# Kernel tuning notes

Measured on AMD Instinct MI355X. Metric: run time of the kernel, lower is better.

Reference implementation:

```python
import jax, jax.numpy as jnp
import numpy as np

N_NODES = 50000
N_EDGES = 400000
N_GRAPHS = 128
IN_DIM = 768
HID = 128
N_CLASSES = 11
BN_EPS = 1e-5


def _sage_conv(x, src, dst, Wl, bl, Wr):
    # PyG SAGEConv (aggr='mean'): out = lin_l(mean_{j->i} x_j) + lin_r(x_i)
    # messages flow src -> dst; nodes with no in-edges get a zero aggregate.
    n = x.shape[0]
    deg = jax.ops.segment_sum(jnp.ones_like(dst, x.dtype), dst, num_segments=n)
    agg = jax.ops.segment_sum(x[src], dst, num_segments=n)  # [N, d] gather+scatter
    agg = agg / jnp.maximum(deg, 1.0)[:, None]
    return agg @ Wl.T + bl + x @ Wr.T


def _batch_norm(x, gamma, beta):
    # training-mode BatchNorm1d: biased batch statistics over the node axis
    m = jnp.mean(x, axis=0)
    v = jnp.var(x, axis=0)
    return (x - m) * jax.lax.rsqrt(v + BN_EPS) * gamma + beta


def setup_inputs() -> dict:
    key = jax.random.key(0)
    ks = jax.random.split(key, 16)
    x = jax.random.normal(ks[0], (N_NODES, IN_DIM), dtype=jnp.float32)
    edge_index = jax.random.randint(ks[1], (2, N_EDGES), 0, N_NODES, dtype=jnp.int32)
    batch = jnp.sort(jax.random.randint(ks[2], (N_NODES,), 0, N_GRAPHS, dtype=jnp.int32))

    def lin_w(k, out_d, in_d):
        return jax.random.normal(k, (out_d, in_d), dtype=jnp.float32) * (1.0 / np.sqrt(in_d))

    params = {
        'W1l': lin_w(ks[3], HID, IN_DIM), 'b1': jnp.zeros((HID,), jnp.float32),
        'W1r': lin_w(ks[4], HID, IN_DIM),
        'g1': jnp.ones((HID,), jnp.float32), 'be1': jnp.zeros((HID,), jnp.float32),
        'W2l': lin_w(ks[5], HID, HID), 'b2': jnp.zeros((HID,), jnp.float32),
        'W2r': lin_w(ks[6], HID, HID),
        'g2': jnp.ones((HID,), jnp.float32), 'be2': jnp.zeros((HID,), jnp.float32),
        'W3l': lin_w(ks[7], HID, HID), 'b3': jnp.zeros((HID,), jnp.float32),
        'W3r': lin_w(ks[8], HID, HID),
        'g3': jnp.ones((HID,), jnp.float32), 'be3': jnp.zeros((HID,), jnp.float32),
        'Wlin': lin_w(ks[9], N_CLASSES, HID), 'blin': jnp.zeros((N_CLASSES,), jnp.float32),
    }
    return {'x': x, 'edge_index': edge_index, 'batch': batch, **params}


def reference(x, edge_index, batch,
              W1l, b1, W1r, g1, be1,
              W2l, b2, W2r, g2, be2,
              W3l, b3, W3r, g3, be3,
              Wlin, blin):
    src, dst = edge_index[0], edge_index[1]
    h = jax.nn.relu(_batch_norm(_sage_conv(x, src, dst, W1l, b1, W1r), g1, be1))
    h = jax.nn.relu(_batch_norm(_sage_conv(h, src, dst, W2l, b2, W2r), g2, be2))
    h = _batch_norm(_sage_conv(h, src, dst, W3l, b3, W3r), g3, be3)
    # global_max_pool over graph ids
    pooled = jax.ops.segment_max(h, batch, num_segments=N_GRAPHS)  # [G, HID]
    # dropout is identity at inference
    return pooled @ Wlin.T + blin  # [G, 11]
```

## Files before the change

### kernel.cpp

```cpp
#include <hip/hip_runtime.h>

#define N_NODESC 50000
#define N_EDGESC 400000
#define N_GRAPHSC 128
#define IN_DIMC 768
#define HIDC 128
#define NCLSC 11
#define BN_EPSC 1e-5f
#define NB_AGG 8
#define NREP 64
#define SCAN_NB ((N_NODESC + 255) / 256)

typedef __bf16 bf16_t;
typedef __bf16 bf16x2 __attribute__((ext_vector_type(2)));
typedef __bf16 bf16x8 __attribute__((ext_vector_type(8)));
typedef float f32x4 __attribute__((ext_vector_type(4)));

typedef __attribute__((address_space(1))) void glb_void;
typedef __attribute__((address_space(3))) void lds_void;

__device__ __forceinline__ void cp16(const void* g, void* l) {
    __builtin_amdgcn_global_load_lds((glb_void*)g, (lds_void*)l, 16, 0, 0);
}

__device__ __forceinline__ f32x4 mfma_16x16x32_bf16(bf16x8 a, bf16x8 b, f32x4 c) {
    return __builtin_amdgcn_mfma_f32_16x16x32_bf16(a, b, c, 0, 0, 0);
}

template<int MODE, int KC>
__global__ __launch_bounds__(256) void gemm_kernel(const void* __restrict__ Av,
                                                   const bf16_t* __restrict__ Wb,
                                                   const float* __restrict__ stats,
                                                   const float* __restrict__ g,
                                                   const float* __restrict__ be,
                                                   bf16_t* __restrict__ Cl,
                                                   bf16_t* __restrict__ Cr,
                                                   int M)
{
    constexpr int NK   = KC / 32;
    constexpr int ASZ  = (MODE == 0) ? 16384 : 8192;
    constexpr int BSZ  = 8192;
    constexpr int NAB  = (MODE == 0) ? 2 : 3;
    constexpr int NBB  = (MODE == 0) ? 2 : 3;
    constexpr int AISS = (MODE == 0) ? 4 : 2;
    constexpr int SCSZ = (MODE == 1) ? 1024 : 16;
    __shared__ __align__(16) unsigned char smem[NAB * ASZ + NBB * BSZ + SCSZ];
    unsigned char* Asm = smem;
    unsigned char* Bsm = smem + NAB * ASZ;
    float* scS = (float*)(smem + NAB * ASZ + NBB * BSZ);

    const int bid  = blockIdx.x;
    const int p    = ((bid >> 4) << 3) + (bid & 7);
    const int half = (bid >> 3) & 1;
    if (p * 128 >= M) return;
    const int m0 = p * 128;

    const int t    = threadIdx.x;
    const int wid  = t >> 6;
    const int lane = t & 63;
    const int wm   = (wid >> 1) * 64;
    const int wn   = (wid & 1) * 64;
    const int l16  = lane & 15;
    const int quad = lane >> 4;

    const char* aSrc[AISS]; int aDst[AISS];
#pragma unroll
    for (int s = 0; s < AISS; s++) {
        int L = (s * 4 + wid) * 64 + lane;
        int r, c;
        if (MODE == 0) { r = L >> 3; c = (L & 7) ^ (r & 7); }
        else           { r = L >> 2; c = (L & 3) ^ ((r >> 1) & 3); }
        int row = m0 + r; if (row > M - 1) row = M - 1;
        if (MODE == 0) aSrc[s] = (const char*)Av + ((size_t)row * KC + (size_t)c * 4) * 4;
        else           aSrc[s] = (const char*)Av + ((size_t)row * KC + (size_t)c * 8) * 2;
        aDst[s] = (s * 4 + wid) * 1024;
    }
    const char* bSrc[2]; int bDst[2];
#pragma unroll
    for (int s = 0; s < 2; s++) {
        int L = (s * 4 + wid) * 64 + lane;
        int r = L >> 2;
        int c = (L & 3) ^ ((r >> 1) & 3);
        bSrc[s] = (const char*)(Wb + (size_t)(half * 128 + r) * KC + c * 8);
        bDst[s] = (s * 4 + wid) * 1024;
    }

    int aOff[4][2], bOff[4];
#pragma unroll
    for (int i = 0; i < 4; i++) {
        int ra = wm + i * 16 + l16;
        if (MODE == 0) {
            aOff[i][0] = ra * 128 + (((2 * quad)     ^ (ra & 7)) * 16);
            aOff[i][1] = ra * 128 + (((2 * quad + 1) ^ (ra & 7)) * 16);
        } else {
            aOff[i][0] = ra * 64 + ((quad ^ ((ra >> 1) & 3)) * 16);
            aOff[i][1] = 0;
        }
        int rb = wn + i * 16 + l16;
        bOff[i] = rb * 64 + ((quad ^ ((rb >> 1) & 3)) * 16);
    }

    if (MODE == 1) {
        if (t < HIDC) {
            float sum = 0.f, sumsq = 0.f;
            for (int r = 0; r < NREP; r++) {
                sum   += stats[r * 256 + t];
                sumsq += stats[r * 256 + HIDC + t];
            }
            float invM = 1.0f / (float)M;
            float mean = sum * invM;
            float var  = sumsq * invM - mean * mean;
            float s = rsqrtf(var + BN_EPSC) * g[t];
            scS[t] = s;
            scS[HIDC + t] = be[t] - mean * s;
        }
        __syncthreads();
    }

    f32x4 acc[4][4] = {};

    if constexpr (MODE == 0) {
#pragma unroll
        for (int s = 0; s < 4; s++) cp16(aSrc[s], Asm + aDst[s]);
#pragma unroll
        for (int s = 0; s < 2; s++) cp16(bSrc[s], Bsm + bDst[s]);

        for (int it = 0; it < NK; ++it) {
            if (it + 1 < NK) {
                const size_t ka = (size_t)(it + 1) * 128;
                const size_t kb = (size_t)(it + 1) * 64;
                const int nb = (it + 1) & 1;
#pragma unroll
                for (int s = 0; s < 4; s++) cp16(aSrc[s] + ka, Asm + nb * ASZ + aDst[s]);
#pragma unroll
                for (int s = 0; s < 2; s++) cp16(bSrc[s] + kb, Bsm + nb * BSZ + bDst[s]);
                asm volatile("s_waitcnt vmcnt(6)" ::: "memory");
            } else {
                asm volatile("s_waitcnt vmcnt(0)" ::: "memory");
            }
            asm volatile("s_barrier" ::: "memory");

            const unsigned char* Ab = Asm + (it & 1) * ASZ;
            const unsigned char* Bb = Bsm + (it & 1) * BSZ;
            bf16x8 af[4], bfr[4];
#pragma unroll
            for (int i = 0; i < 4; i++) {
                float4 u0 = *(const float4*)(Ab + aOff[i][0]);
                float4 u1 = *(const float4*)(Ab + aOff[i][1]);
                af[i][0] = (bf16_t)u0.x; af[i][1] = (bf16_t)u0.y;
                af[i][2] = (bf16_t)u0.z; af[i][3] = (bf16_t)u0.w;
                af[i][4] = (bf16_t)u1.x; af[i][5] = (bf16_t)u1.y;
                af[i][6] = (bf16_t)u1.z; af[i][7] = (bf16_t)u1.w;
            }
#pragma unroll
            for (int j = 0; j < 4; j++)
                bfr[j] = *(const bf16x8*)(Bb + bOff[j]);
#pragma unroll
            for (int i = 0; i < 4; i++)
#pragma unroll
                for (int j = 0; j < 4; j++)
                    acc[i][j] = mfma_16x16x32_bf16(af[i], bfr[j], acc[i][j]);

            asm volatile("s_barrier" ::: "memory");
        }
    } else {
#pragma unroll
        for (int s = 0; s < 2; s++) cp16(aSrc[s], Asm + aDst[s]);
#pragma unroll
        for (int s = 0; s < 2; s++) cp16(bSrc[s], Bsm + bDst[s]);
#pragma unroll
        for (int s = 0; s < 2; s++) cp16(aSrc[s] + 64, Asm + ASZ + aDst[s]);
#pragma unroll
        for (int s = 0; s < 2; s++) cp16(bSrc[s] + 64, Bsm + BSZ + bDst[s]);

        for (int it = 0; it < NK; ++it) {
            if (it + 2 < NK) {
                const size_t kb2 = (size_t)(it + 2) * 64;
                const int nb = (it + 2) % 3;
#pragma unroll
                for (int s = 0; s < 2; s++) cp16(aSrc[s] + kb2, Asm + nb * ASZ + aDst[s]);
#pragma unroll
                for (int s = 0; s < 2; s++) cp16(bSrc[s] + kb2, Bsm + nb * BSZ + bDst[s]);
                asm volatile("s_waitcnt vmcnt(8)" ::: "memory");
            } else if (it + 1 < NK) {
                asm volatile("s_waitcnt vmcnt(4)" ::: "memory");
            } else {
                asm volatile("s_waitcnt vmcnt(0)" ::: "memory");
            }
            asm volatile("s_barrier" ::: "memory");

            const unsigned char* Ab = Asm + (it % 3) * ASZ;
            const unsigned char* Bb = Bsm + (it % 3) * BSZ;
            bf16x8 af[4], bfr[4];
            float4 s0 = *(const float4*)&scS[it * 32 + quad * 8];
            float4 s1 = *(const float4*)&scS[it * 32 + quad * 8 + 4];
            float4 h0 = *(const float4*)&scS[HIDC + it * 32 + quad * 8];
            float4 h1 = *(const float4*)&scS[HIDC + it * 32 + quad * 8 + 4];
            float ss[8] = {s0.x, s0.y, s0.z, s0.w, s1.x, s1.y, s1.z, s1.w};
            float hh[8] = {h0.x, h0.y, h0.z, h0.w, h1.x, h1.y, h1.z, h1.w};
#pragma unroll
            for (int i = 0; i < 4; i++) {
                bf16x8 raw = *(const bf16x8*)(Ab + aOff[i][0]);
#pragma unroll
                for (int e = 0; e < 8; e++)
                    af[i][e] = (bf16_t)fmaxf(fmaf((float)raw[e], ss[e], hh[e]), 0.0f);
            }
#pragma unroll
            for (int j = 0; j < 4; j++)
                bfr[j] = *(const bf16x8*)(Bb + bOff[j]);
#pragma unroll
            for (int i = 0; i < 4; i++)
#pragma unroll
                for (int j = 0; j < 4; j++)
                    acc[i][j] = mfma_16x16x32_bf16(af[i], bfr[j], acc[i][j]);

            asm volatile("s_barrier" ::: "memory");
        }
    }

    bf16_t* C = half ? Cr : Cl;
#pragma unroll
    for (int i = 0; i < 4; i++) {
        int rowb = m0 + wm + i * 16 + quad * 4;
#pragma unroll
        for (int j = 0; j < 4; j++) {
            int colh = wn + j * 16 + l16;
#pragma unroll
            for (int rr = 0; rr < 4; rr++) {
                int row = rowb + rr;
                if (row < M) C[(size_t)row * HIDC + colh] = (bf16_t)acc[i][j][rr];
            }
        }
    }
}

__global__ void init_kernel(const float* __restrict__ W1l, const float* __restrict__ W1r,
                            const float* __restrict__ W2l, const float* __restrict__ W2r,
                            const float* __restrict__ W3l, const float* __restrict__ W3r,
                            bf16_t* __restrict__ Wb1, bf16_t* __restrict__ Wb2,
                            bf16_t* __restrict__ Wb3,
                            int* __restrict__ degi, float* __restrict__ stats)
{
    const int NW1 = 128 * IN_DIMC;
    const int NW2 = 128 * HIDC;
    const int NS  = 3 * NREP * 256;
    int j = blockIdx.x * blockDim.x + threadIdx.x;
    if (j < 2 * NW1) { Wb1[j] = (bf16_t)((j < NW1) ? W1l[j] : W1r[j - NW1]); return; }
    j -= 2 * NW1;
    if (j < 2 * NW2) { Wb2[j] = (bf16_t)((j < NW2) ? W2l[j] : W2r[j - NW2]); return; }
    j -= 2 * NW2;
    if (j < 2 * NW2) { Wb3[j] = (bf16_t)((j < NW2) ? W3l[j] : W3r[j - NW2]); return; }
    j -= 2 * NW2;
    if (j < NS) { stats[j] = 0.0f; return; }
    j -= NS;
    if (j < N_NODESC) degi[j] = 0;
}

__global__ void degi_kernel(const int* __restrict__ ei, int* __restrict__ degi) {
    int e = blockIdx.x * blockDim.x + threadIdx.x;
    if (e < N_EDGESC) atomicAdd(&degi[ei[N_EDGESC + e]], 1);
}

__global__ __launch_bounds__(256) void scan1_kernel(const int* __restrict__ degi,
                                                    int* __restrict__ local,
                                                    int* __restrict__ partials)
{
    __shared__ int tmp[256];
    const int t = threadIdx.x;
    const int i = blockIdx.x * 256 + t;
    int v = (i < N_NODESC) ? degi[i] : 0;
    tmp[t] = v;
    __syncthreads();
    for (int off = 1; off < 256; off <<= 1) {
        int u = (t >= off) ? tmp[t - off] : 0;
        __syncthreads();
        tmp[t] += u;
        __syncthreads();
    }
    if (i < N_NODESC) local[i] = tmp[t] - v;
    if (t == 255) partials[blockIdx.x] = tmp[255];
}

__global__ __launch_bounds__(256) void scan3_kernel(const int* __restrict__ local,
                                                    const int* __restrict__ partials,
                                                    int* __restrict__ rowptr,
                                                    int* __restrict__ cursor)
{
    __shared__ int inc[256];
    __shared__ int orig[256];
    const int t = threadIdx.x;
    int v = (t < SCAN_NB) ? partials[t] : 0;
    inc[t] = v; orig[t] = v;
    __syncthreads();
    for (int off = 1; off < 256; off <<= 1) {
        int u = (t >= off) ? inc[t - off] : 0;
        __syncthreads();
        inc[t] += u;
        __syncthreads();
    }
    const int boff = inc[blockIdx.x] - orig[blockIdx.x];
    const int i = blockIdx.x * 256 + t;
    if (i < N_NODESC) {
        int r = local[i] + boff;
        rowptr[i] = r;
        cursor[i] = r;
    }
    if (i == 0) rowptr[N_NODESC] = N_EDGESC;
}

__global__ void fill_kernel(const int* __restrict__ ei, int* __restrict__ cursor,
                            int* __restrict__ col) {
    int e = blockIdx.x * blockDim.x + threadIdx.x;
    if (e >= N_EDGESC) return;
    int d = ei[N_EDGESC + e];
    int pos = atomicAdd(&cursor[d], 1);
    col[pos] = ei[e];
}

__global__ __launch_bounds__(128) void agg_combine_kernel(const int* __restrict__ rowptr,
                                                          const int* __restrict__ col,
                                                          const bf16_t* __restrict__ Plb,
                                                          const bf16_t* __restrict__ Prb,
                                                          const float* __restrict__ bias,
                                                          bf16_t* __restrict__ Hb,
                                                          float* __restrict__ stats, int M)
{
    const int lane = threadIdx.x & 63;
    const int wv   = threadIdx.x >> 6;
    const int c0   = lane * 2;
    const float b0 = bias[c0], b1v = bias[c0 + 1];
    float s0 = 0.f, s1 = 0.f, q0 = 0.f, q1 = 0.f;
    const int n0 = blockIdx.x * NB_AGG + wv * (NB_AGG / 2);
    for (int rr = 0; rr < NB_AGG / 2; rr++) {
        int n = n0 + rr;
        if (n >= M) break;
        int lo = rowptr[n], hi = rowptr[n + 1];
        float a0 = 0.f, a1 = 0.f;
        for (int e = lo; e < hi; e += 8) {
            int rem = hi - e;
            int idx[8];
#pragma unroll
            for (int j = 0; j < 8; j++) {
                int ee = e + j; if (ee > hi - 1) ee = hi - 1;
                idx[j] = col[ee];
            }
            bf16x2 v[8];
#pragma unroll
            for (int j = 0; j < 8; j++)
                v[j] = *(const bf16x2*)&Plb[(size_t)idx[j] * HIDC + c0];
#pragma unroll
            for (int j = 0; j < 8; j++)
                if (j < rem) { a0 += (float)v[j][0]; a1 += (float)v[j][1]; }
        }
        int d = hi - lo;
        float inv = 1.0f / (float)(d > 0 ? d : 1);
        bf16x2 pr = *(const bf16x2*)&Prb[(size_t)n * HIDC + c0];
        float pre0 = fmaf(a0, inv, b0) + (float)pr[0];
        float pre1 = fmaf(a1, inv, b1v) + (float)pr[1];
        bf16x2 hv; hv[0] = (bf16_t)pre0; hv[1] = (bf16_t)pre1;
        *(bf16x2*)&Hb[(size_t)n * HIDC + c0] = hv;
        s0 += pre0; s1 += pre1; q0 += pre0 * pre0; q1 += pre1 * pre1;
    }
    const int rep = (blockIdx.x * 2 + wv) & (NREP - 1);
    atomicAdd(&stats[rep * 256 + c0], s0);
    atomicAdd(&stats[rep * 256 + c0 + 1], s1);
    atomicAdd(&stats[rep * 256 + HIDC + c0], q0);
    atomicAdd(&stats[rep * 256 + HIDC + c0 + 1], q1);
}

__global__ __launch_bounds__(128) void poolhead_kernel(const bf16_t* __restrict__ Hb,
                                                       const float* __restrict__ stats,
                                                       const float* __restrict__ g,
                                                       const float* __restrict__ be,
                                                       const int* __restrict__ batch,
                                                       const float* __restrict__ Wlin,
                                                       const float* __restrict__ blin,
                                                       float* __restrict__ out, int M)
{
    __shared__ float sp[HIDC];
    int gph = blockIdx.x;
    int c   = threadIdx.x;
    float sum = 0.f, sumsq = 0.f;
    for (int r = 0; r < NREP; r++) {
        sum   += stats[r * 256 + c];
        sumsq += stats[r * 256 + HIDC + c];
    }
    float invM = 1.0f / (float)M;
    float mean = sum * invM;
    float var  = sumsq * invM - mean * mean;
    float s = rsqrtf(var + BN_EPSC) * g[c];
    float h = be[c] - mean * s;

    int lo = 0, hi = M;
    while (lo < hi) { int m = (lo + hi) >> 1; if (batch[m] < gph) lo = m + 1; else hi = m; }
    int lo2 = lo, hi2 = M;
    while (lo2 < hi2) { int m = (lo2 + hi2) >> 1; if (batch[m] < gph + 1) lo2 = m + 1; else hi2 = m; }
    float mx = -INFINITY;
    for (int rr = lo; rr < lo2; rr++)
        mx = fmaxf(mx, fmaf((float)Hb[(size_t)rr * HIDC + c], s, h));
    sp[c] = mx;
    __syncthreads();
    if (c < NCLSC) {
        float acc = blin[c];
        for (int k = 0; k < HIDC; k++) acc += sp[k] * Wlin[c * HIDC + k];
        out[gph * NCLSC + c] = acc;
    }
}

extern "C" void kernel_launch(void* const* d_in, const int* in_sizes, int n_in,
                              void* d_out, int out_size, void* d_ws, size_t ws_size,
                              hipStream_t stream)
{
    const float* x     = (const float*)d_in[0];
    const int*   ei    = (const int*)d_in[1];
    const int*   batch = (const int*)d_in[2];
    const float* W1l = (const float*)d_in[3];
    const float* b1  = (const float*)d_in[4];
    const float* W1r = (const float*)d_in[5];
    const float* g1  = (const float*)d_in[6];
    const float* be1 = (const float*)d_in[7];
    const float* W2l = (const float*)d_in[8];
    const float* b2  = (const float*)d_in[9];
    const float* W2r = (const float*)d_in[10];
    const float* g2  = (const float*)d_in[11];
    const float* be2 = (const float*)d_in[12];
    const float* W3l = (const float*)d_in[13];
    const float* b3  = (const float*)d_in[14];
    const float* W3r = (const float*)d_in[15];
    const float* g3  = (const float*)d_in[16];
    const float* be3 = (const float*)d_in[17];
    const float* Wlin = (const float*)d_in[18];
    const float* blin = (const float*)d_in[19];

    const int M = N_NODESC;

    char* w = (char*)d_ws;
    bf16_t* Plb  = (bf16_t*)w;  w += (size_t)M * HIDC * 2;
    bf16_t* Prb  = (bf16_t*)w;  w += (size_t)M * HIDC * 2;
    bf16_t* Hb   = (bf16_t*)w;  w += (size_t)M * HIDC * 2;
    bf16_t* Wb1  = (bf16_t*)w;  w += (size_t)256 * IN_DIMC * 2;
    bf16_t* Wb2  = (bf16_t*)w;  w += (size_t)256 * HIDC * 2;
    bf16_t* Wb3  = (bf16_t*)w;  w += (size_t)256 * HIDC * 2;
    int*   rowptr= (int*)w;     w += (size_t)(M + 16) * 4;
    int*   col   = (int*)w;     w += (size_t)N_EDGESC * 4;
    int*   cursor= (int*)w;     w += (size_t)M * 4;
    int*   degi  = (int*)w;     w += (size_t)M * 4;
    int*   slocal= (int*)w;     w += (size_t)M * 4;
    int*   spart = (int*)w;     w += 256 * 4;
    float* stats = (float*)w;   w += (size_t)3 * NREP * 256 * 4;

    float* stats1 = stats;
    float* stats2 = stats + NREP * 256;
    float* stats3 = stats + 2 * NREP * 256;

    const int nP = (M + 127) / 128;
    const dim3 gemm_grid(((nP + 7) / 8) * 16);
    const int agg_blocks = (M + NB_AGG - 1) / NB_AGG;
    const int init_total = 2 * 128 * IN_DIMC + 4 * 128 * HIDC + 3 * NREP * 256 + M;

    init_kernel<<<(init_total + 255) / 256, 256, 0, stream>>>(W1l, W1r, W2l, W2r, W3l, W3r,
                                                              Wb1, Wb2, Wb3, degi, stats);
    degi_kernel<<<(N_EDGESC + 255) / 256, 256, 0, stream>>>(ei, degi);
    scan1_kernel<<<SCAN_NB, 256, 0, stream>>>(degi, slocal, spart);
    scan3_kernel<<<SCAN_NB, 256, 0, stream>>>(slocal, spart, rowptr, cursor);
    fill_kernel<<<(N_EDGESC + 255) / 256, 256, 0, stream>>>(ei, cursor, col);

    gemm_kernel<0, IN_DIMC><<<gemm_grid, 256, 0, stream>>>(x, Wb1, nullptr, nullptr, nullptr,
                                                           Plb, Prb, M);
    agg_combine_kernel<<<agg_blocks, 128, 0, stream>>>(rowptr, col, Plb, Prb, b1, Hb, stats1, M);

    gemm_kernel<1, HIDC><<<gemm_grid, 256, 0, stream>>>(Hb, Wb2, stats1, g1, be1, Plb, Prb, M);
    agg_combine_kernel<<<agg_blocks, 128, 0, stream>>>(rowptr, col, Plb, Prb, b2, Hb, stats2, M);

    gemm_kernel<1, HIDC><<<gemm_grid, 256, 0, stream>>>(Hb, Wb3, stats2, g2, be2, Plb, Prb, M);
    agg_combine_kernel<<<agg_blocks, 128, 0, stream>>>(rowptr, col, Plb, Prb, b3, Hb, stats3, M);

    poolhead_kernel<<<N_GRAPHSC, 128, 0, stream>>>(Hb, stats3, g3, be3, batch, Wlin, blin,
                                                   (float*)d_out, M);
}
```

Measured before the change: 581.9 us.

## Compute full 256-wide layer-1 output per block and interleave 4-node aggregation gathers

The layer-1 GEMM now has each block compute both the left and right projections (N=256) for a 128-row tile. Before, two blocks each loaded the same fp32 x tile, so this halves global reads of the large 768-wide input. The cost is more accumulator registers and 64KB of LDS per block, with a 2-block occupancy hint. The aggregation kernel also processes four nodes per wave at once, issuing their neighbor gathers together to raise memory-level parallelism, at the cost of more registers and extra wasted lanes on degree imbalance.

```diff
diff --git a/kernel.cpp b/kernel.cpp
--- a/kernel.cpp
+++ b/kernel.cpp
@@ -27,27 +27,141 @@
     return __builtin_amdgcn_mfma_f32_16x16x32_bf16(a, b, c, 0, 0, 0);
 }
 
-template<int MODE, int KC>
-__global__ __launch_bounds__(256) void gemm_kernel(const void* __restrict__ Av,
-                                                   const bf16_t* __restrict__ Wb,
-                                                   const float* __restrict__ stats,
-                                                   const float* __restrict__ g,
-                                                   const float* __restrict__ be,
-                                                   bf16_t* __restrict__ Cl,
-                                                   bf16_t* __restrict__ Cr,
-                                                   int M)
-{
-    constexpr int NK   = KC / 32;
-    constexpr int ASZ  = (MODE == 0) ? 16384 : 8192;
-    constexpr int BSZ  = 8192;
-    constexpr int NAB  = (MODE == 0) ? 2 : 3;
-    constexpr int NBB  = (MODE == 0) ? 2 : 3;
-    constexpr int AISS = (MODE == 0) ? 4 : 2;
-    constexpr int SCSZ = (MODE == 1) ? 1024 : 16;
-    __shared__ __align__(16) unsigned char smem[NAB * ASZ + NBB * BSZ + SCSZ];
+__global__ __launch_bounds__(256, 2) void gemm_l1_kernel(const float* __restrict__ Av,
+                                                         const bf16_t* __restrict__ Wb,
+                                                         bf16_t* __restrict__ Cl,
+                                                         bf16_t* __restrict__ Cr,
+                                                         int M)
+{
+    constexpr int KC  = IN_DIMC;
+    constexpr int NK  = KC / 32;
+    constexpr int ASZ = 16384;
+    constexpr int BSZ = 16384;
+    __shared__ __align__(16) unsigned char smem[2 * ASZ + 2 * BSZ];
     unsigned char* Asm = smem;
-    unsigned char* Bsm = smem + NAB * ASZ;
-    float* scS = (float*)(smem + NAB * ASZ + NBB * BSZ);
+    unsigned char* Bsm = smem + 2 * ASZ;
+
+    const int m0   = blockIdx.x * 128;
+    const int t    = threadIdx.x;
+    const int wid  = t >> 6;
+    const int lane = t & 63;
+    const int wm   = (wid >> 1) * 64;
+    const int l16  = lane & 15;
+    const int quad = lane >> 4;
+
+    const char* aSrc[4]; int aDst[4];
+#pragma unroll
+    for (int s = 0; s < 4; s++) {
+        int L = (s * 4 + wid) * 64 + lane;
+        int r = L >> 3;
+        int c = (L & 7) ^ (r & 7);
+        int row = m0 + r; if (row > M - 1) row = M - 1;
+        aSrc[s] = (const char*)Av + ((size_t)row * KC + (size_t)c * 4) * 4;
+        aDst[s] = (s * 4 + wid) * 1024;
+    }
+    const char* bSrc[4]; int bDst[4];
+#pragma unroll
+    for (int s = 0; s < 4; s++) {
+        int L = (s * 4 + wid) * 64 + lane;
+        int r = L >> 2;
+        int c = (L & 3) ^ ((r >> 1) & 3);
+        bSrc[s] = (const char*)(Wb + (size_t)r * KC + c * 8);
+        bDst[s] = (s * 4 + wid) * 1024;
+    }
+
+    int aOff[4][2], bOff[8];
+#pragma unroll
+    for (int i = 0; i < 4; i++) {
+        int ra = wm + i * 16 + l16;
+        aOff[i][0] = ra * 128 + (((2 * quad)     ^ (ra & 7)) * 16);
+        aOff[i][1] = ra * 128 + (((2 * quad + 1) ^ (ra & 7)) * 16);
+    }
+    const int wnb = (wid & 1) * 128;
+#pragma unroll
+    for (int j = 0; j < 8; j++) {
+        int rb = wnb + j * 16 + l16;
+        bOff[j] = rb * 64 + ((quad ^ ((rb >> 1) & 3)) * 16);
+    }
+
+    f32x4 acc[4][8] = {};
+
+#pragma unroll
+    for (int s = 0; s < 4; s++) cp16(aSrc[s], Asm + aDst[s]);
+#pragma unroll
+    for (int s = 0; s < 4; s++) cp16(bSrc[s], Bsm + bDst[s]);
+
+    for (int it = 0; it < NK; ++it) {
+        if (it + 1 < NK) {
+            const size_t ka = (size_t)(it + 1) * 128;
+            const size_t kb = (size_t)(it + 1) * 64;
+            const int nb = (it + 1) & 1;
+#pragma unroll
+            for (int s = 0; s < 4; s++) cp16(aSrc[s] + ka, Asm + nb * ASZ + aDst[s]);
+#pragma unroll
+            for (int s = 0; s < 4; s++) cp16(bSrc[s] + kb, Bsm + nb * BSZ + bDst[s]);
+            asm volatile("s_waitcnt vmcnt(8)" ::: "memory");
+        } else {
+            asm volatile("s_waitcnt vmcnt(0)" ::: "memory");
+        }
+        asm volatile("s_barrier" ::: "memory");
+
+        const unsigned char* Ab = Asm + (it & 1) * ASZ;
+        const unsigned char* Bb = Bsm + (it & 1) * BSZ;
+        bf16x8 af[4], bfr[8];
+#pragma unroll
+        for (int i = 0; i < 4; i++) {
+            float4 u0 = *(const float4*)(Ab + aOff[i][0]);
+            float4 u1 = *(const float4*)(Ab + aOff[i][1]);
+            af[i][0] = (bf16_t)u0.x; af[i][1] = (bf16_t)u0.y;
+            af[i][2] = (bf16_t)u0.z; af[i][3] = (bf16_t)u0.w;
+            af[i][4] = (bf16_t)u1.x; af[i][5] = (bf16_t)u1.y;
+            af[i][6] = (bf16_t)u1.z; af[i][7] = (bf16_t)u1.w;
+        }
+#pragma unroll
+        for (int j = 0; j < 8; j++)
+            bfr[j] = *(const bf16x8*)(Bb + bOff[j]);
+#pragma unroll
+        for (int i = 0; i < 4; i++)
+#pragma unroll
+            for (int j = 0; j < 8; j++)
+                acc[i][j] = mfma_16x16x32_bf16(af[i], bfr[j], acc[i][j]);
+
+        asm volatile("s_barrier" ::: "memory");
+    }
+
+    bf16_t* C = (wid & 1) ? Cr : Cl;
+#pragma unroll
+    for (int i = 0; i < 4; i++) {
+        int rowb = m0 + wm + i * 16 + quad * 4;
+#pragma unroll
+        for (int j = 0; j < 8; j++) {
+            int colh = j * 16 + l16;
+#pragma unroll
+            for (int rr = 0; rr < 4; rr++) {
+                int row = rowb + rr;
+                if (row < M) C[(size_t)row * HIDC + colh] = (bf16_t)acc[i][j][rr];
+            }
+        }
+    }
+}
+
+__global__ __launch_bounds__(256) void gemm_hid_kernel(const bf16_t* __restrict__ Av,
+                                                       const bf16_t* __restrict__ Wb,
+                                                       const float* __restrict__ stats,
+                                                       const float* __restrict__ g,
+                                                       const float* __restrict__ be,
+                                                       bf16_t* __restrict__ Cl,
+                                                       bf16_t* __restrict__ Cr,
+                                                       int M)
+{
+    constexpr int KC  = HIDC;
+    constexpr int NK  = KC / 32;
+    constexpr int ASZ = 8192;
+    constexpr int BSZ = 8192;
+    __shared__ __align__(16) unsigned char smem[3 * ASZ + 3 * BSZ + 1024];
+    unsigned char* Asm = smem;
+    unsigned char* Bsm = smem + 3 * ASZ;
+    float* scS = (float*)(smem + 3 * ASZ + 3 * BSZ);
 
     const int bid  = blockIdx.x;
     const int p    = ((bid >> 4) << 3) + (bid & 7);
@@ -63,18 +177,6 @@
     const int l16  = lane & 15;
     const int quad = lane >> 4;
 
-    const char* aSrc[AISS]; int aDst[AISS];
-#pragma unroll
-    for (int s = 0; s < AISS; s++) {
-        int L = (s * 4 + wid) * 64 + lane;
-        int r, c;
-        if (MODE == 0) { r = L >> 3; c = (L & 7) ^ (r & 7); }
-        else           { r = L >> 2; c = (L & 3) ^ ((r >> 1) & 3); }
-        int row = m0 + r; if (row > M - 1) row = M - 1;
-        if (MODE == 0) aSrc[s] = (const char*)Av + ((size_t)row * KC + (size_t)c * 4) * 4;
-        else           aSrc[s] = (const char*)Av + ((size_t)row * KC + (size_t)c * 8) * 2;
-        aDst[s] = (s * 4 + wid) * 1024;
-    }
     const char* bSrc[2]; int bDst[2];
 #pragma unroll
     for (int s = 0; s < 2; s++) {
@@ -84,138 +186,94 @@
         bSrc[s] = (const char*)(Wb + (size_t)(half * 128 + r) * KC + c * 8);
         bDst[s] = (s * 4 + wid) * 1024;
     }
-
-    int aOff[4][2], bOff[4];
+    const char* aSrc[2]; int aDst[2];
+#pragma unroll
+    for (int s = 0; s < 2; s++) {
+        int L = (s * 4 + wid) * 64 + lane;
+        int r = L >> 2;
+        int c = (L & 3) ^ ((r >> 1) & 3);
+        int row = m0 + r; if (row > M - 1) row = M - 1;
+        aSrc[s] = (const char*)Av + ((size_t)row * KC + (size_t)c * 8) * 2;
+        aDst[s] = (s * 4 + wid) * 1024;
+    }
+
+    int aOff[4], bOff[4];
 #pragma unroll
     for (int i = 0; i < 4; i++) {
         int ra = wm + i * 16 + l16;
-        if (MODE == 0) {
-            aOff[i][0] = ra * 128 + (((2 * quad)     ^ (ra & 7)) * 16);
-            aOff[i][1] = ra * 128 + (((2 * quad + 1) ^ (ra & 7)) * 16);
-        } else {
-            aOff[i][0] = ra * 64 + ((quad ^ ((ra >> 1) & 3)) * 16);
-            aOff[i][1] = 0;
-        }
+        aOff[i] = ra * 64 + ((quad ^ ((ra >> 1) & 3)) * 16);
         int rb = wn + i * 16 + l16;
         bOff[i] = rb * 64 + ((quad ^ ((rb >> 1) & 3)) * 16);
     }
 
-    if (MODE == 1) {
-        if (t < HIDC) {
-            float sum = 0.f, sumsq = 0.f;
-            for (int r = 0; r < NREP; r++) {
-                sum   += stats[r * 256 + t];
-                sumsq += stats[r * 256 + HIDC + t];
-            }
-            float invM = 1.0f / (float)M;
-            float mean = sum * invM;
-            float var  = sumsq * invM - mean * mean;
-            float s = rsqrtf(var + BN_EPSC) * g[t];
-            scS[t] = s;
-            scS[HIDC + t] = be[t] - mean * s;
-        }
-        __syncthreads();
-    }
+    if (t < HIDC) {
+        float sum = 0.f, sumsq = 0.f;
+        for (int r = 0; r < NREP; r++) {
+            sum   += stats[r * 256 + t];
+            sumsq += stats[r * 256 + HIDC + t];
+        }
+        float invM = 1.0f / (float)M;
+        float mean = sum * invM;
+        float var  = sumsq * invM - mean * mean;
+        float s = rsqrtf(var + BN_EPSC) * g[t];
+        scS[t] = s;
+        scS[HIDC + t] = be[t] - mean * s;
+    }
+    __syncthreads();
 
     f32x4 acc[4][4] = {};
 
-    if constexpr (MODE == 0) {
-#pragma unroll
-        for (int s = 0; s < 4; s++) cp16(aSrc[s], Asm + aDst[s]);
-#pragma unroll
-        for (int s = 0; s < 2; s++) cp16(bSrc[s], Bsm + bDst[s]);
-
-        for (int it = 0; it < NK; ++it) {
-            if (it + 1 < NK) {
-                const size_t ka = (size_t)(it + 1) * 128;
-                const size_t kb = (size_t)(it + 1) * 64;
-                const int nb = (it + 1) & 1;
-#pragma unroll
-                for (int s = 0; s < 4; s++) cp16(aSrc[s] + ka, Asm + nb * ASZ + aDst[s]);
-#pragma unroll
-                for (int s = 0; s < 2; s++) cp16(bSrc[s] + kb, Bsm + nb * BSZ + bDst[s]);
-                asm volatile("s_waitcnt vmcnt(6)" ::: "memory");
-            } else {
-                asm volatile("s_waitcnt vmcnt(0)" ::: "memory");
-            }
-            asm volatile("s_barrier" ::: "memory");
-
-            const unsigned char* Ab = Asm + (it & 1) * ASZ;
-            const unsigned char* Bb = Bsm + (it & 1) * BSZ;
-            bf16x8 af[4], bfr[4];
-#pragma unroll
-            for (int i = 0; i < 4; i++) {
-                float4 u0 = *(const float4*)(Ab + aOff[i][0]);
-                float4 u1 = *(const float4*)(Ab + aOff[i][1]);
-                af[i][0] = (bf16_t)u0.x; af[i][1] = (bf16_t)u0.y;
-                af[i][2] = (bf16_t)u0.z; af[i][3] = (bf16_t)u0.w;
-                af[i][4] = (bf16_t)u1.x; af[i][5] = (bf16_t)u1.y;
-                af[i][6] = (bf16_t)u1.z; af[i][7] = (bf16_t)u1.w;
-            }
+#pragma unroll
+    for (int s = 0; s < 2; s++) cp16(aSrc[s], Asm + aDst[s]);
+#pragma unroll
+    for (int s = 0; s < 2; s++) cp16(bSrc[s], Bsm + bDst[s]);
+#pragma unroll
+    for (int s = 0; s < 2; s++) cp16(aSrc[s] + 64, Asm + ASZ + aDst[s]);
+#pragma unroll
+    for (int s = 0; s < 2; s++) cp16(bSrc[s] + 64, Bsm + BSZ + bDst[s]);
+
+    for (int it = 0; it < NK; ++it) {
+        if (it + 2 < NK) {
+            const size_t kb2 = (size_t)(it + 2) * 64;
+            const int nb = (it + 2) % 3;
+#pragma unroll
+            for (int s = 0; s < 2; s++) cp16(aSrc[s] + kb2, Asm + nb * ASZ + aDst[s]);
+#pragma unroll
+            for (int s = 0; s < 2; s++) cp16(bSrc[s] + kb2, Bsm + nb * BSZ + bDst[s]);
+            asm volatile("s_waitcnt vmcnt(8)" ::: "memory");
+        } else if (it + 1 < NK) {
+            asm volatile("s_waitcnt vmcnt(4)" ::: "memory");
+        } else {
+            asm volatile("s_waitcnt vmcnt(0)" ::: "memory");
+        }
+        asm volatile("s_barrier" ::: "memory");
+
+        const unsigned char* Ab = Asm + (it % 3) * ASZ;
+        const unsigned char* Bb = Bsm + (it % 3) * BSZ;
+        bf16x8 af[4], bfr[4];
+        float4 s0 = *(const float4*)&scS[it * 32 + quad * 8];
+        float4 s1 = *(const float4*)&scS[it * 32 + quad * 8 + 4];
+        float4 h0 = *(const float4*)&scS[HIDC + it * 32 + quad * 8];
+        float4 h1 = *(const float4*)&scS[HIDC + it * 32 + quad * 8 + 4];
+        float ss[8] = {s0.x, s0.y, s0.z, s0.w, s1.x, s1.y, s1.z, s1.w};
+        float hh[8] = {h0.x, h0.y, h0.z, h0.w, h1.x, h1.y, h1.z, h1.w};
+#pragma unroll
+        for (int i = 0; i < 4; i++) {
+            bf16x8 raw = *(const bf16x8*)(Ab + aOff[i]);
+#pragma unroll
+            for (int e = 0; e < 8; e++)
+                af[i][e] = (bf16_t)fmaxf(fmaf((float)raw[e], ss[e], hh[e]), 0.0f);
+        }
+#pragma unroll
+        for (int j = 0; j < 4; j++)
+            bfr[j] = *(const bf16x8*)(Bb + bOff[j]);
+#pragma unroll
+        for (int i = 0; i < 4; i++)
 #pragma unroll
             for (int j = 0; j < 4; j++)
-                bfr[j] = *(const bf16x8*)(Bb + bOff[j]);
-#pragma unroll
-            for (int i = 0; i < 4; i++)
-#pragma unroll
-                for (int j = 0; j < 4; j++)
-                    acc[i][j] = mfma_16x16x32_bf16(af[i], bfr[j], acc[i][j]);
-
-            asm volatile("s_barrier" ::: "memory");
-        }
-    } else {
-#pragma unroll
-        for (int s = 0; s < 2; s++) cp16(aSrc[s], Asm + aDst[s]);
-#pragma unroll
-        for (int s = 0; s < 2; s++) cp16(bSrc[s], Bsm + bDst[s]);
-#pragma unroll
-        for (int s = 0; s < 2; s++) cp16(aSrc[s] + 64, Asm + ASZ + aDst[s]);
-#pragma unroll
-        for (int s = 0; s < 2; s++) cp16(bSrc[s] + 64, Bsm + BSZ + bDst[s]);
-
-        for (int it = 0; it < NK; ++it) {
-            if (it + 2 < NK) {
-                const size_t kb2 = (size_t)(it + 2) * 64;
-                const int nb = (it + 2) % 3;
-#pragma unroll
-                for (int s = 0; s < 2; s++) cp16(aSrc[s] + kb2, Asm + nb * ASZ + aDst[s]);
-#pragma unroll
-                for (int s = 0; s < 2; s++) cp16(bSrc[s] + kb2, Bsm + nb * BSZ + bDst[s]);
-                asm volatile("s_waitcnt vmcnt(8)" ::: "memory");
-            } else if (it + 1 < NK) {
-                asm volatile("s_waitcnt vmcnt(4)" ::: "memory");
-            } else {
-                asm volatile("s_waitcnt vmcnt(0)" ::: "memory");
-            }
-            asm volatile("s_barrier" ::: "memory");
-
-            const unsigned char* Ab = Asm + (it % 3) * ASZ;
-            const unsigned char* Bb = Bsm + (it % 3) * BSZ;
-            bf16x8 af[4], bfr[4];
-            float4 s0 = *(const float4*)&scS[it * 32 + quad * 8];
-            float4 s1 = *(const float4*)&scS[it * 32 + quad * 8 + 4];
-            float4 h0 = *(const float4*)&scS[HIDC + it * 32 + quad * 8];
-            float4 h1 = *(const float4*)&scS[HIDC + it * 32 + quad * 8 + 4];
-            float ss[8] = {s0.x, s0.y, s0.z, s0.w, s1.x, s1.y, s1.z, s1.w};
-            float hh[8] = {h0.x, h0.y, h0.z, h0.w, h1.x, h1.y, h1.z, h1.w};
-#pragma unroll
-            for (int i = 0; i < 4; i++) {
-                bf16x8 raw = *(const bf16x8*)(Ab + aOff[i][0]);
-#pragma unroll
-                for (int e = 0; e < 8; e++)
-                    af[i][e] = (bf16_t)fmaxf(fmaf((float)raw[e], ss[e], hh[e]), 0.0f);
-            }
-#pragma unroll
-            for (int j = 0; j < 4; j++)
-                bfr[j] = *(const bf16x8*)(Bb + bOff[j]);
-#pragma unroll
-            for (int i = 0; i < 4; i++)
-#pragma unroll
-                for (int j = 0; j < 4; j++)
-                    acc[i][j] = mfma_16x16x32_bf16(af[i], bfr[j], acc[i][j]);
-
-            asm volatile("s_barrier" ::: "memory");
-        }
+                acc[i][j] = mfma_16x16x32_bf16(af[i], bfr[j], acc[i][j]);
+
+        asm volatile("s_barrier" ::: "memory");
     }
 
     bf16_t* C = half ? Cr : Cl;
@@ -329,37 +387,73 @@
     const int wv   = threadIdx.x >> 6;
     const int c0   = lane * 2;
     const float b0 = bias[c0], b1v = bias[c0 + 1];
+    const int n0 = blockIdx.x * NB_AGG + wv * (NB_AGG / 2);
+
+    int lo[4], hi[4], pos[4];
+    bf16x2 pr[4];
+#pragma unroll
+    for (int r = 0; r < 4; r++) {
+        int n = n0 + r;
+        lo[r] = (n < M) ? rowptr[n] : 0;
+        hi[r] = (n < M) ? rowptr[n + 1] : 0;
+        pos[r] = lo[r];
+        if (n < M) pr[r] = *(const bf16x2*)&Prb[(size_t)n * HIDC + c0];
+        else { pr[r][0] = (bf16_t)0.f; pr[r][1] = (bf16_t)0.f; }
+    }
+
+    float a0[4] = {0.f, 0.f, 0.f, 0.f}, a1[4] = {0.f, 0.f, 0.f, 0.f};
+
+    for (;;) {
+        int cnt[4];
+        bool any = false;
+#pragma unroll
+        for (int r = 0; r < 4; r++) {
+            int c = hi[r] - pos[r];
+            cnt[r] = (c > 8) ? 8 : c;
+            if (cnt[r] > 0) any = true;
+        }
+        if (!any) break;
+
+        bf16x2 v[4][8];
+#pragma unroll
+        for (int r = 0; r < 4; r++) {
+            if (cnt[r] > 0) {
+                int idx[8];
+#pragma unroll
+                for (int j = 0; j < 8; j++) {
+                    int ee = pos[r] + j;
+                    if (ee > hi[r] - 1) ee = hi[r] - 1;
+                    idx[j] = col[ee];
+                }
+#pragma unroll
+                for (int j = 0; j < 8; j++)
+                    v[r][j] = *(const bf16x2*)&Plb[(size_t)idx[j] * HIDC + c0];
+            }
+        }
+#pragma unroll
+        for (int r = 0; r < 4; r++) {
+            if (cnt[r] > 0) {
+#pragma unroll
+                for (int j = 0; j < 8; j++)
+                    if (j < cnt[r]) { a0[r] += (float)v[r][j][0]; a1[r] += (float)v[r][j][1]; }
+                pos[r] += cnt[r];
+            }
+        }
+    }
+
     float s0 = 0.f, s1 = 0.f, q0 = 0.f, q1 = 0.f;
-    const int n0 = blockIdx.x * NB_AGG + wv * (NB_AGG / 2);
-    for (int rr = 0; rr < NB_AGG / 2; rr++) {
-        int n = n0 + rr;
-        if (n >= M) break;
-        int lo = rowptr[n], hi = rowptr[n + 1];
-        float a0 = 0.f, a1 = 0.f;
-        for (int e = lo; e < hi; e += 8) {
-            int rem = hi - e;
-            int idx[8];
-#pragma unroll
-            for (int j = 0; j < 8; j++) {
-                int ee = e + j; if (ee > hi - 1) ee = hi - 1;
-                idx[j] = col[ee];
-            }
-            bf16x2 v[8];
-#pragma unroll
-            for (int j = 0; j < 8; j++)
-                v[j] = *(const bf16x2*)&Plb[(size_t)idx[j] * HIDC + c0];
-#pragma unroll
-            for (int j = 0; j < 8; j++)
-                if (j < rem) { a0 += (float)v[j][0]; a1 += (float)v[j][1]; }
-        }
-        int d = hi - lo;
-        float inv = 1.0f / (float)(d > 0 ? d : 1);
-        bf16x2 pr = *(const bf16x2*)&Prb[(size_t)n * HIDC + c0];
-        float pre0 = fmaf(a0, inv, b0) + (float)pr[0];
-        float pre1 = fmaf(a1, inv, b1v) + (float)pr[1];
-        bf16x2 hv; hv[0] = (bf16_t)pre0; hv[1] = (bf16_t)pre1;
-        *(bf16x2*)&Hb[(size_t)n * HIDC + c0] = hv;
-        s0 += pre0; s1 += pre1; q0 += pre0 * pre0; q1 += pre1 * pre1;
+#pragma unroll
+    for (int r = 0; r < 4; r++) {
+        int n = n0 + r;
+        if (n < M) {
+            int d = hi[r] - lo[r];
+            float inv = 1.0f / (float)(d > 0 ? d : 1);
+            float pre0 = fmaf(a0[r], inv, b0) + (float)pr[r][0];
+            float pre1 = fmaf(a1[r], inv, b1v) + (float)pr[r][1];
+            bf16x2 hv; hv[0] = (bf16_t)pre0; hv[1] = (bf16_t)pre1;
+            *(bf16x2*)&Hb[(size_t)n * HIDC + c0] = hv;
+            s0 += pre0; s1 += pre1; q0 += pre0 * pre0; q1 += pre1 * pre1;
+        }
     }
     const int rep = (blockIdx.x * 2 + wv) & (NREP - 1);
     atomicAdd(&stats[rep * 256 + c0], s0);
@@ -454,7 +548,8 @@
     float* stats3 = stats + 2 * NREP * 256;
 
     const int nP = (M + 127) / 128;
-    const dim3 gemm_grid(((nP + 7) / 8) * 16);
+    const dim3 l1_grid(nP);
+    const dim3 hid_grid(((nP + 7) / 8) * 16);
     const int agg_blocks = (M + NB_AGG - 1) / NB_AGG;
     const int init_total = 2 * 128 * IN_DIMC + 4 * 128 * HIDC + 3 * NREP * 256 + M;
 
@@ -465,14 +560,13 @@
     scan3_kernel<<<SCAN_NB, 256, 0, stream>>>(slocal, spart, rowptr, cursor);
     fill_kernel<<<(N_EDGESC + 255) / 256, 256, 0, stream>>>(ei, cursor, col);
 
-    gemm_kernel<0, IN_DIMC><<<gemm_grid, 256, 0, stream>>>(x, Wb1, nullptr, nullptr, nullptr,
-                                                           Plb, Prb, M);
+    gemm_l1_kernel<<<l1_grid, 256, 0, stream>>>(x, Wb1, Plb, Prb, M);
     agg_combine_kernel<<<agg_blocks, 128, 0, stream>>>(rowptr, col, Plb, Prb, b1, Hb, stats1, M);
 
-    gemm_kernel<1, HIDC><<<gemm_grid, 256, 0, stream>>>(Hb, Wb2, stats1, g1, be1, Plb, Prb, M);
+    gemm_hid_kernel<<<hid_grid, 256, 0, stream>>>(Hb, Wb2, stats1, g1, be1, Plb, Prb, M);
     agg_combine_kernel<<<agg_blocks, 128, 0, stream>>>(rowptr, col, Plb, Prb, b2, Hb, stats2, M);
 
-    gemm_kernel<1, HIDC><<<gemm_grid, 256, 0, stream>>>(Hb, Wb3, stats2, g2, be2, Plb, Prb, M);
+    gemm_hid_kernel<<<hid_grid, 256, 0, stream>>>(Hb, Wb3, stats2, g2, be2, Plb, Prb, M);
     agg_combine_kernel<<<agg_blocks, 128, 0, stream>>>(rowptr, col, Plb, Prb, b3, Hb, stats3, M);
 
     poolhead_kernel<<<N_GRAPHSC, 128, 0, stream>>>(Hb, stats3, g3, be3, batch, Wlin, blin,
```

New measurement: 556.8 us. -4.3%, faster.
